# Kernel optimization log

Measured on AMD Instinct MI355X. Metric: run time of the kernel, lower is better.

## Reference

```python
import jax, jax.numpy as jnp
import numpy as np

K = 24
D = 128
BETA = 0.5
DECAY = 0.95
TEMP = 1.0  # temp_start; module uses self.temperature which starts at temp_start
B = 524288


def setup_inputs() -> dict:
    key = jax.random.key(0)
    k1, k2, k3, k4, k5 = jax.random.split(key, 5)
    z_e = jax.random.normal(k1, (B, D), dtype=jnp.float32)
    # nn.init.uniform_(codebook.weight, -1/K, 1/K)
    codebook = jax.random.uniform(k2, (K, D), dtype=jnp.float32,
                                  minval=-1.0 / K, maxval=1.0 / K)
    # buffers: cluster sizes in [0, 2) so some fall below the 0.1 dead threshold
    ema_cluster_size = jax.random.uniform(k3, (K,), dtype=jnp.float32) * 2.0
    ema_embedding_sum = jax.random.normal(k4, (K, D), dtype=jnp.float32) * 0.1
    rand_idx = jax.random.randint(k5, (K,), 0, B)  # restart sources, worst case n_dead=K
    return {
        "z_e": z_e,
        "codebook": codebook,
        "ema_cluster_size": ema_cluster_size,
        "ema_embedding_sum": ema_embedding_sum,
        "rand_idx": rand_idx,
    }


def reference(z_e, codebook, ema_cluster_size, ema_embedding_sum, rand_idx):
    # squared L2 distances [B, K]: ||z||^2 - 2 z.W^T + ||w||^2
    dists = (jnp.sum(z_e * z_e, axis=1, keepdims=True)
             - 2.0 * (z_e @ codebook.T)
             + jnp.sum(codebook * codebook, axis=1))
    indices = jnp.argmin(dists, axis=1)          # [B]
    z_q_hard = codebook[indices]                 # [B, D]

    # training path: Gumbel-softmax style soft assignment (softmax over -d/T)
    weights = jax.nn.softmax(-dists / TEMP, axis=1)   # [B, K]
    z_q_soft = weights @ codebook                     # [B, D]

    # ---- EMA codebook update (no-grad in the original) ----
    ones = jnp.ones((z_e.shape[0],), dtype=z_e.dtype)
    new_cluster_size = jax.ops.segment_sum(ones, indices, num_segments=K)     # one_hot.sum(0)
    new_embedding_sum = jax.ops.segment_sum(z_e, indices, num_segments=K)     # one_hot.T @ z_e
    ecs = DECAY * ema_cluster_size + (1.0 - DECAY) * new_cluster_size
    ees = DECAY * ema_embedding_sum + (1.0 - DECAY) * new_embedding_sum
    n = jnp.sum(ecs)
    smoothed = (ecs + 1e-5) / (n + K * 1e-5) * n
    codebook_new = ees / smoothed[:, None]

    # dead-code restart: rows with ecs < 0.1 get a random z_e row
    dead = ecs < 0.1                         # [K] bool
    restart = z_e[rand_idx]                  # [K, D]
    codebook_new = jnp.where(dead[:, None], restart, codebook_new)
    ecs = jnp.where(dead, jnp.asarray(1.0, ecs.dtype), ecs)
    ees = jnp.where(dead[:, None], restart, ees)

    # ---- VQ loss ----
    loss_codebook = jnp.mean((z_q_hard - jax.lax.stop_gradient(z_e)) ** 2)
    loss_commit = jnp.mean((z_e - jax.lax.stop_gradient(z_q_hard)) ** 2)
    loss_vq = loss_codebook + BETA * loss_commit

    return (z_q_soft, z_q_hard, indices, weights, loss_vq,
            codebook_new, ecs, ees)
```

## Files before the change

kernel.cpp:

```cpp
#include <hip/hip_runtime.h>

#define KC 24
#define DC 128
#define TPB 256
#define NROWS 524288
#define CBS 132
#define WSTR 28
#define NSLICE 8

#define NB_EBIN 1024
#define ROWS_PER_EBIN (NROWS / NB_EBIN)
#define PSTR 3104
#define FINAL_OFF (NB_EBIN * PSTR)
#define LOSS_OFF (FINAL_OFF + PSTR)
#define RB 32

typedef float vfloat2 __attribute__((ext_vector_type(2)));
typedef float vfloat4 __attribute__((ext_vector_type(4)));

__device__ __forceinline__ void nt_store2(float* p, float x, float y) {
    vfloat2 v; v.x = x; v.y = y;
    __builtin_nontemporal_store(v, (vfloat2*)p);
}
__device__ __forceinline__ void nt_store4(float* p, float4 q) {
    vfloat4 v; v.x = q.x; v.y = q.y; v.z = q.z; v.w = q.w;
    __builtin_nontemporal_store(v, (vfloat4*)p);
}

__global__ void vq_zero(float* __restrict__ acc) {
    int i = blockIdx.x * blockDim.x + threadIdx.x;
    if (i < PSTR + NSLICE) acc[FINAL_OFF + i] = 0.0f;
}

__global__ __launch_bounds__(TPB, 4) void vq_main(
    const float* __restrict__ z_e, const float* __restrict__ cb,
    float* __restrict__ o_soft, float* __restrict__ o_hard,
    float* __restrict__ o_idx, float* __restrict__ o_w,
    float* __restrict__ acc)
{
    __shared__ float cb_s[KC][CBS];
    __shared__ float wn_s[KC];
    __shared__ float w_s[4][64][WSTR];
    __shared__ int   idx_s[TPB];

    const int tid = threadIdx.x;
    const int wv  = tid >> 6;
    const int l   = tid & 63;

    #pragma unroll 1
    for (int i = tid; i < KC * DC; i += TPB)
        cb_s[i >> 7][i & (DC - 1)] = cb[i];
    __syncthreads();
    if (tid < KC) {
        float s = 0.0f;
        #pragma unroll 1
        for (int d = 0; d < DC; ++d) s = fmaf(cb_s[tid][d], cb_s[tid][d], s);
        wn_s[tid] = s;
    }
    __syncthreads();

    const int row = blockIdx.x * TPB + tid;
    const float* zp = z_e + (size_t)row * DC;

    float dv[KC];
    #pragma unroll
    for (int k = 0; k < KC; ++k) dv[k] = 0.0f;
    float zn = 0.0f;

    #pragma unroll 1
    for (int c = 0; c < 4; ++c) {
        float4 a[8];
        #pragma unroll
        for (int i = 0; i < 8; ++i)
            a[i] = *(const float4*)(zp + c * 32 + 4 * i);
        #pragma unroll
        for (int i = 0; i < 8; ++i)
            zn = fmaf(a[i].x, a[i].x, fmaf(a[i].y, a[i].y,
                 fmaf(a[i].z, a[i].z, fmaf(a[i].w, a[i].w, zn))));
        #pragma unroll
        for (int k = 0; k < KC; ++k) {
            float s = dv[k];
            #pragma unroll
            for (int i = 0; i < 8; ++i) {
                const float4 wvv = *(const float4*)(&cb_s[k][c * 32 + 4 * i]);
                s = fmaf(a[i].x, wvv.x, fmaf(a[i].y, wvv.y,
                    fmaf(a[i].z, wvv.z, fmaf(a[i].w, wvv.w, s))));
            }
            dv[k] = s;
        }
    }

    int idx = 0;
    float best = 3.4e38f;
    #pragma unroll
    for (int k = 0; k < KC; ++k) {
        float d = (zn - 2.0f * dv[k]) + wn_s[k];
        dv[k] = d;
        if (d < best) { best = d; idx = k; }
    }
    float ssum = 0.0f;
    #pragma unroll
    for (int k = 0; k < KC; ++k) {
        float e = __expf(best - dv[k]);
        dv[k] = e;
        ssum += e;
    }
    const float inv = 1.0f / ssum;
    #pragma unroll
    for (int k = 0; k < KC; ++k) dv[k] *= inv;

    #pragma unroll
    for (int q = 0; q < 6; ++q)
        *(float4*)(&w_s[wv][l][4 * q]) =
            make_float4(dv[4*q], dv[4*q+1], dv[4*q+2], dv[4*q+3]);
    idx_s[tid] = idx;
    o_idx[row] = (float)idx;

    {
        float loss_acc = best;
        #pragma unroll
        for (int off = 32; off > 0; off >>= 1)
            loss_acc += __shfl_down(loss_acc, off);
        if (l == 0)
            atomicAdd(acc + LOSS_OFF + (blockIdx.x & (NSLICE - 1)), loss_acc);
    }
    __syncthreads();

    const int base2 = blockIdx.x * TPB + wv * 64;
    float2 cbr[KC];
    #pragma unroll
    for (int k = 0; k < KC; ++k)
        cbr[k] = *(const float2*)(&cb_s[k][2 * l]);

    #pragma unroll 2
    for (int j = 0; j < 64; ++j) {
        const int r = base2 + j;
        const int ic = idx_s[wv * 64 + j];
        float wk[KC];
        #pragma unroll
        for (int q = 0; q < 6; ++q) {
            const float4 wq = *(const float4*)(&w_s[wv][j][4 * q]);
            wk[4*q+0] = wq.x; wk[4*q+1] = wq.y;
            wk[4*q+2] = wq.z; wk[4*q+3] = wq.w;
        }
        float q0 = 0.0f, q1 = 0.0f;
        #pragma unroll
        for (int k = 0; k < KC; ++k) {
            q0 = fmaf(wk[k], cbr[k].x, q0);
            q1 = fmaf(wk[k], cbr[k].y, q1);
        }
        nt_store2(o_soft + (size_t)r * DC + 2 * l, q0, q1);
        const float2 h2 = *(const float2*)(&cb_s[ic][2 * l]);
        nt_store2(o_hard + (size_t)r * DC + 2 * l, h2.x, h2.y);
    }

    #pragma unroll
    for (int i = 0; i < 6; ++i) {
        const int fo = i * 64 + l;
        const int jr = fo / 6, c = fo % 6;
        const float4 v = *(const float4*)(&w_s[wv][jr][4 * c]);
        nt_store4(o_w + (size_t)base2 * KC + 4 * fo, v);
    }
}

__global__ __launch_bounds__(TPB) void vq_ebin(
    const float* __restrict__ z_e, const float* __restrict__ o_idx,
    float* __restrict__ acc)
{
    __shared__ float eb[4][KC][DC];
    __shared__ float cnt_sh[4][KC];

    const int tid = threadIdx.x;
    const int w   = tid >> 6;
    const int l   = tid & 63;
    const int d2  = 2 * l;

    #pragma unroll 1
    for (int i = l; i < KC * DC / 2; i += 64)
        ((float2*)&eb[w][0][0])[i] = make_float2(0.0f, 0.0f);
    if (l < KC) cnt_sh[w][l] = 0.0f;

    const int r0 = blockIdx.x * ROWS_PER_EBIN + w * (ROWS_PER_EBIN / 4);

    #pragma unroll 1
    for (int rb = 0; rb < ROWS_PER_EBIN / 4; rb += 16) {
        float2 v[16];
        float  fid[16];
        #pragma unroll
        for (int j = 0; j < 16; ++j)
            v[j] = *(const float2*)(z_e + (size_t)(r0 + rb + j) * DC + d2);
        #pragma unroll
        for (int j = 0; j < 16; ++j)
            fid[j] = o_idx[r0 + rb + j];
        #pragma unroll
        for (int j = 0; j < 16; ++j) {
            const int ic = (int)fid[j];
            float2 cur = *(float2*)(&eb[w][ic][d2]);
            cur.x += v[j].x;
            cur.y += v[j].y;
            *(float2*)(&eb[w][ic][d2]) = cur;
            if (l == 0) cnt_sh[w][ic] += 1.0f;
        }
    }
    __syncthreads();

    float* part = acc + (size_t)blockIdx.x * PSTR;
    #pragma unroll 1
    for (int i = tid; i < KC * DC; i += TPB) {
        const int k = i >> 7, d = i & (DC - 1);
        part[i] = (eb[0][k][d] + eb[1][k][d]) + (eb[2][k][d] + eb[3][k][d]);
    }
    if (tid < KC)
        part[KC * DC + tid] = (cnt_sh[0][tid] + cnt_sh[1][tid])
                            + (cnt_sh[2][tid] + cnt_sh[3][tid]);
}

__global__ void vq_reduce(float* __restrict__ acc) {
    const int i = blockIdx.x * blockDim.x + threadIdx.x;
    if (i >= KC * DC + KC) return;
    const int b0 = blockIdx.y * RB;
    float s0 = 0.0f, s1 = 0.0f, s2 = 0.0f, s3 = 0.0f;
    #pragma unroll 2
    for (int b = b0; b < b0 + RB; b += 4) {
        s0 += acc[(size_t)(b + 0) * PSTR + i];
        s1 += acc[(size_t)(b + 1) * PSTR + i];
        s2 += acc[(size_t)(b + 2) * PSTR + i];
        s3 += acc[(size_t)(b + 3) * PSTR + i];
    }
    atomicAdd(&acc[FINAL_OFF + i], (s0 + s1) + (s2 + s3));
}

__global__ void vq_epilogue(
    const float* __restrict__ z_e, const float* __restrict__ ema_cs,
    const float* __restrict__ ema_es, const int* __restrict__ rand_idx,
    const float* __restrict__ acc,
    float* __restrict__ o_loss, float* __restrict__ o_cbn,
    float* __restrict__ o_ecs, float* __restrict__ o_ees)
{
    __shared__ float ecs_s[KC], sm_s[KC];
    __shared__ float n_sh;
    const int tid = threadIdx.x;
    const float* fin = acc + FINAL_OFF;
    if (tid < KC)
        ecs_s[tid] = 0.95f * ema_cs[tid] + 0.05f * fin[KC * DC + tid];
    __syncthreads();
    if (tid == 0) {
        float n = 0.0f;
        for (int k = 0; k < KC; ++k) n += ecs_s[k];
        n_sh = n;
    }
    __syncthreads();
    if (tid < KC) {
        float n = n_sh;
        sm_s[tid] = (ecs_s[tid] + 1e-5f) / (n + (float)KC * 1e-5f) * n;
    }
    __syncthreads();
    #pragma unroll 1
    for (int i = tid; i < KC * DC; i += TPB) {
        int k = i >> 7, d = i & (DC - 1);
        float ees = 0.95f * ema_es[i] + 0.05f * fin[i];
        float cbn = ees / sm_s[k];
        bool dead = ecs_s[k] < 0.1f;
        float rst = z_e[(size_t)rand_idx[k] * DC + d];
        o_cbn[i] = dead ? rst : cbn;
        o_ees[i] = dead ? rst : ees;
    }
    if (tid < KC) o_ecs[tid] = (ecs_s[tid] < 0.1f) ? 1.0f : ecs_s[tid];
    if (tid == 0) {
        float lsum = 0.0f;
        #pragma unroll
        for (int s = 0; s < NSLICE; ++s) lsum += acc[LOSS_OFF + s];
        o_loss[0] = 1.5f * (lsum * (1.0f / 67108864.0f));
    }
}

extern "C" void kernel_launch(void* const* d_in, const int* in_sizes, int n_in,
                              void* d_out, int out_size, void* d_ws, size_t ws_size,
                              hipStream_t stream) {
    const float* z_e    = (const float*)d_in[0];
    const float* cb     = (const float*)d_in[1];
    const float* ema_cs = (const float*)d_in[2];
    const float* ema_es = (const float*)d_in[3];
    const int*   ridx   = (const int*)d_in[4];

    float* out = (float*)d_out;
    float* o_soft = out;
    float* o_hard = out + 67108864ll;
    float* o_idx  = out + 134217728ll;
    float* o_w    = out + 134742016ll;
    float* o_loss = out + 147324928ll;
    float* o_cbn  = out + 147324929ll;
    float* o_ecs  = out + 147328001ll;
    float* o_ees  = out + 147328025ll;

    float* acc = (float*)d_ws;

    vq_zero<<<(PSTR + NSLICE + TPB - 1) / TPB, TPB, 0, stream>>>(acc);
    vq_main<<<NROWS / TPB, TPB, 0, stream>>>(
        z_e, cb, o_soft, o_hard, o_idx, o_w, acc);
    vq_ebin<<<NB_EBIN, TPB, 0, stream>>>(z_e, o_idx, acc);
    {
        dim3 g((KC * DC + KC + TPB - 1) / TPB, NB_EBIN / RB);
        vq_reduce<<<g, TPB, 0, stream>>>(acc);
    }
    vq_epilogue<<<1, TPB, 0, stream>>>(
        z_e, ema_cs, ema_es, ridx, acc, o_loss, o_cbn, o_ecs, o_ees);
}
```

Measured before the change: 297.8 us.

## Fuse per-cluster embedding-sum binning into main VQ kernel via shared-memory slots

Removes the separate vq_ebin kernel, which re-read all of z_e and the index output. Each vq_main block now reuses its weights shared buffer to accumulate the per-cluster z_e sums and counts for its 256 rows. It then atomically adds them into one of 1024 workspace slots, which are zeroed up front. This saves a full pass over z_e (256 MB) and a kernel launch. The cost is extra syncthreads, serialized per-wave accumulation in the main kernel, global atomics, and a larger zeroing kernel.

```diff
diff --git a/kernel.cpp b/kernel.cpp
--- a/kernel.cpp
+++ b/kernel.cpp
@@ -8,12 +8,13 @@
 #define WSTR 28
 #define NSLICE 8
 
-#define NB_EBIN 1024
-#define ROWS_PER_EBIN (NROWS / NB_EBIN)
+#define NSLOT 1024
 #define PSTR 3104
-#define FINAL_OFF (NB_EBIN * PSTR)
+#define FINAL_OFF (NSLOT * PSTR)
 #define LOSS_OFF (FINAL_OFF + PSTR)
+#define ZTOT (LOSS_OFF + NSLICE)
 #define RB 32
+#define U_FLOATS (4 * 64 * WSTR)
 
 typedef float vfloat2 __attribute__((ext_vector_type(2)));
 typedef float vfloat4 __attribute__((ext_vector_type(4)));
@@ -29,7 +30,7 @@
 
 __global__ void vq_zero(float* __restrict__ acc) {
     int i = blockIdx.x * blockDim.x + threadIdx.x;
-    if (i < PSTR + NSLICE) acc[FINAL_OFF + i] = 0.0f;
+    if (i < ZTOT) acc[i] = 0.0f;
 }
 
 __global__ __launch_bounds__(TPB, 4) void vq_main(
@@ -40,12 +41,13 @@
 {
     __shared__ float cb_s[KC][CBS];
     __shared__ float wn_s[KC];
-    __shared__ float w_s[4][64][WSTR];
+    __shared__ float u_s[U_FLOATS];
     __shared__ int   idx_s[TPB];
 
     const int tid = threadIdx.x;
     const int wv  = tid >> 6;
     const int l   = tid & 63;
+    const int d2  = 2 * l;
 
     #pragma unroll 1
     for (int i = tid; i < KC * DC; i += TPB)
@@ -61,6 +63,7 @@
 
     const int row = blockIdx.x * TPB + tid;
     const float* zp = z_e + (size_t)row * DC;
+    float* wsp = &u_s[wv * 64 * WSTR];
 
     float dv[KC];
     #pragma unroll
@@ -111,7 +114,7 @@
 
     #pragma unroll
     for (int q = 0; q < 6; ++q)
-        *(float4*)(&w_s[wv][l][4 * q]) =
+        *(float4*)(&wsp[l * WSTR + 4 * q]) =
             make_float4(dv[4*q], dv[4*q+1], dv[4*q+2], dv[4*q+3]);
     idx_s[tid] = idx;
     o_idx[row] = (float)idx;
@@ -130,7 +133,7 @@
     float2 cbr[KC];
     #pragma unroll
     for (int k = 0; k < KC; ++k)
-        cbr[k] = *(const float2*)(&cb_s[k][2 * l]);
+        cbr[k] = *(const float2*)(&cb_s[k][d2]);
 
     #pragma unroll 2
     for (int j = 0; j < 64; ++j) {
@@ -139,7 +142,7 @@
         float wk[KC];
         #pragma unroll
         for (int q = 0; q < 6; ++q) {
-            const float4 wq = *(const float4*)(&w_s[wv][j][4 * q]);
+            const float4 wq = *(const float4*)(&wsp[j * WSTR + 4 * q]);
             wk[4*q+0] = wq.x; wk[4*q+1] = wq.y;
             wk[4*q+2] = wq.z; wk[4*q+3] = wq.w;
         }
@@ -149,70 +152,52 @@
             q0 = fmaf(wk[k], cbr[k].x, q0);
             q1 = fmaf(wk[k], cbr[k].y, q1);
         }
-        nt_store2(o_soft + (size_t)r * DC + 2 * l, q0, q1);
-        const float2 h2 = *(const float2*)(&cb_s[ic][2 * l]);
-        nt_store2(o_hard + (size_t)r * DC + 2 * l, h2.x, h2.y);
+        nt_store2(o_soft + (size_t)r * DC + d2, q0, q1);
+        const float2 h2 = *(const float2*)(&cb_s[ic][d2]);
+        nt_store2(o_hard + (size_t)r * DC + d2, h2.x, h2.y);
     }
 
     #pragma unroll
     for (int i = 0; i < 6; ++i) {
         const int fo = i * 64 + l;
         const int jr = fo / 6, c = fo % 6;
-        const float4 v = *(const float4*)(&w_s[wv][jr][4 * c]);
+        const float4 v = *(const float4*)(&wsp[jr * WSTR + 4 * c]);
         nt_store4(o_w + (size_t)base2 * KC + 4 * fo, v);
     }
-}
-
-__global__ __launch_bounds__(TPB) void vq_ebin(
-    const float* __restrict__ z_e, const float* __restrict__ o_idx,
-    float* __restrict__ acc)
-{
-    __shared__ float eb[4][KC][DC];
-    __shared__ float cnt_sh[4][KC];
-
-    const int tid = threadIdx.x;
-    const int w   = tid >> 6;
-    const int l   = tid & 63;
-    const int d2  = 2 * l;
-
-    #pragma unroll 1
-    for (int i = l; i < KC * DC / 2; i += 64)
-        ((float2*)&eb[w][0][0])[i] = make_float2(0.0f, 0.0f);
-    if (l < KC) cnt_sh[w][l] = 0.0f;
-
-    const int r0 = blockIdx.x * ROWS_PER_EBIN + w * (ROWS_PER_EBIN / 4);
-
-    #pragma unroll 1
-    for (int rb = 0; rb < ROWS_PER_EBIN / 4; rb += 16) {
-        float2 v[16];
-        float  fid[16];
-        #pragma unroll
-        for (int j = 0; j < 16; ++j)
-            v[j] = *(const float2*)(z_e + (size_t)(r0 + rb + j) * DC + d2);
-        #pragma unroll
-        for (int j = 0; j < 16; ++j)
-            fid[j] = o_idx[r0 + rb + j];
-        #pragma unroll
-        for (int j = 0; j < 16; ++j) {
-            const int ic = (int)fid[j];
-            float2 cur = *(float2*)(&eb[w][ic][d2]);
-            cur.x += v[j].x;
-            cur.y += v[j].y;
-            *(float2*)(&eb[w][ic][d2]) = cur;
-            if (l == 0) cnt_sh[w][ic] += 1.0f;
-        }
-    }
-    __syncthreads();
-
-    float* part = acc + (size_t)blockIdx.x * PSTR;
-    #pragma unroll 1
-    for (int i = tid; i < KC * DC; i += TPB) {
-        const int k = i >> 7, d = i & (DC - 1);
-        part[i] = (eb[0][k][d] + eb[1][k][d]) + (eb[2][k][d] + eb[3][k][d]);
-    }
-    if (tid < KC)
-        part[KC * DC + tid] = (cnt_sh[0][tid] + cnt_sh[1][tid])
-                            + (cnt_sh[2][tid] + cnt_sh[3][tid]);
+    __syncthreads();
+
+    #pragma unroll 1
+    for (int i = tid; i < KC * DC + KC; i += TPB) u_s[i] = 0.0f;
+    __syncthreads();
+
+    #pragma unroll 1
+    for (int t = 0; t < 4; ++t) {
+        if (wv == t) {
+            #pragma unroll 1
+            for (int jb = 0; jb < 64; jb += 16) {
+                float2 zv[16];
+                #pragma unroll
+                for (int j = 0; j < 16; ++j)
+                    zv[j] = *(const float2*)(z_e
+                            + (size_t)(base2 + jb + j) * DC + d2);
+                #pragma unroll
+                for (int j = 0; j < 16; ++j) {
+                    const int ic = idx_s[wv * 64 + jb + j];
+                    float2 cur = *(float2*)&u_s[ic * DC + d2];
+                    cur.x += zv[j].x;
+                    cur.y += zv[j].y;
+                    *(float2*)&u_s[ic * DC + d2] = cur;
+                    if (l == 0) u_s[KC * DC + ic] += 1.0f;
+                }
+            }
+        }
+        __syncthreads();
+    }
+
+    float* slot = acc + (size_t)(blockIdx.x & (NSLOT - 1)) * PSTR;
+    #pragma unroll 1
+    for (int i = tid; i < KC * DC + KC; i += TPB)
+        atomicAdd(&slot[i], u_s[i]);
 }
 
 __global__ void vq_reduce(float* __restrict__ acc) {
@@ -295,12 +280,11 @@
 
     float* acc = (float*)d_ws;
 
-    vq_zero<<<(PSTR + NSLICE + TPB - 1) / TPB, TPB, 0, stream>>>(acc);
+    vq_zero<<<(ZTOT + TPB - 1) / TPB, TPB, 0, stream>>>(acc);
     vq_main<<<NROWS / TPB, TPB, 0, stream>>>(
         z_e, cb, o_soft, o_hard, o_idx, o_w, acc);
-    vq_ebin<<<NB_EBIN, TPB, 0, stream>>>(z_e, o_idx, acc);
     {
-        dim3 g((KC * DC + KC + TPB - 1) / TPB, NB_EBIN / RB);
+        dim3 g((KC * DC + KC + TPB - 1) / TPB, NSLOT / RB);
         vq_reduce<<<g, TPB, 0, stream>>>(acc);
     }
     vq_epilogue<<<1, TPB, 0, stream>>>(
```

After: 353.7 us. 18.8% more time.
